# Optimization experiments

Measured on AMD Instinct MI355X. Metric: run time of the kernel, lower is better.

Reference implementation:

```python
import jax, jax.numpy as jnp
import numpy as np

N = 10000
NEG_SLOPE = 0.2

def _glorot(key, shape):
    fan = shape[0] + shape[-1]
    return jax.random.normal(key, shape, dtype=jnp.float32) * jnp.sqrt(2.0 / fan)

def gat_conv(x, src, dst, W, a_src, a_dst, b, heads, ch, concat, n):
    # PyG GATConv: linear (no bias), per-head attention logits, softmax over
    # incoming edges of each target node, weighted scatter-sum, final bias.
    h = (x @ W).reshape(n, heads, ch)                     # [N,H,C]
    al_s = jnp.einsum('nhc,hc->nh', h, a_src)             # [N,H]
    al_d = jnp.einsum('nhc,hc->nh', h, a_dst)
    e = jax.nn.leaky_relu(al_s[src] + al_d[dst], NEG_SLOPE)  # [E,H]
    emax = jax.ops.segment_max(e, dst, num_segments=n)    # [N,H]
    emax = jnp.where(jnp.isfinite(emax), emax, 0.0)
    p = jnp.exp(e - emax[dst])
    denom = jax.ops.segment_sum(p, dst, num_segments=n)   # [N,H]
    alpha = p / (denom[dst] + 1e-16)                      # [E,H]
    out = jax.ops.segment_sum(h[src] * alpha[:, :, None], dst, num_segments=n)
    out = out.reshape(n, heads * ch) if concat else out.mean(axis=1)
    return out + b

def _with_self_loops(edge_index, n):
    loop = jnp.arange(n, dtype=edge_index.dtype)
    src = jnp.concatenate([edge_index[0], loop])
    dst = jnp.concatenate([edge_index[1], loop])
    return src, dst

def setup_inputs() -> dict:
    key = jax.random.key(0)
    ks = jax.random.split(key, 20)
    in_dim, out_dim, E = 128, 256, 160000
    x = jax.random.normal(ks[0], (N, in_dim), dtype=jnp.float32)
    edge_index = jax.random.randint(ks[1], (2, E), 0, N, dtype=jnp.int64)
    return {
        'x': x, 'edge_index': edge_index,
        # conv1: GATConv(128, 256, heads=4, concat=True)
        'W1': _glorot(ks[2], (in_dim, 4 * 256)),
        'a1s': _glorot(ks[3], (4, 256)), 'a1d': _glorot(ks[4], (4, 256)),
        'b1': jnp.zeros((1024,), jnp.float32),
        'S1w': _glorot(ks[5], (in_dim, 1024)), 'S1b': jnp.zeros((1024,), jnp.float32),
        # conv2: GATConv(1024, 256, heads=4, concat=True)
        'W2': _glorot(ks[6], (1024, 4 * 256)),
        'a2s': _glorot(ks[7], (4, 256)), 'a2d': _glorot(ks[8], (4, 256)),
        'b2': jnp.zeros((1024,), jnp.float32),
        'S2w': _glorot(ks[9], (1024, 1024)), 'S2b': jnp.zeros((1024,), jnp.float32),
        # conv3: GATConv(1024, 256, heads=6, concat=False)
        'W3': _glorot(ks[10], (1024, 6 * out_dim)),
        'a3s': _glorot(ks[11], (6, out_dim)), 'a3d': _glorot(ks[12], (6, out_dim)),
        'b3': jnp.zeros((out_dim,), jnp.float32),
        'S3w': _glorot(ks[13], (1024, out_dim)), 'S3b': jnp.zeros((out_dim,), jnp.float32),
    }

def reference(x, edge_index, W1, a1s, a1d, b1, S1w, S1b,
              W2, a2s, a2d, b2, S2w, S2b,
              W3, a3s, a3d, b3, S3w, S3b):
    src, dst = _with_self_loops(edge_index, N)
    h = jax.nn.elu(gat_conv(x, src, dst, W1, a1s, a1d, b1, 4, 256, True, N) + x @ S1w + S1b)
    h = jax.nn.elu(gat_conv(h, src, dst, W2, a2s, a2d, b2, 4, 256, True, N) + h @ S2w + S2b)
    out = gat_conv(h, src, dst, W3, a3s, a3d, b3, 6, 256, False, N) + h @ S3w + S3b
    return out
```

## Files before the change

### kernel.cpp

```cpp
#include <hip/hip_runtime.h>
#include <cfloat>
#include <cmath>
#include <cstdint>

#define NN 10000
#define EE 160000
#define ETOT 170000
#define MPAD 10112

typedef _Float16 f16;
typedef __attribute__((ext_vector_type(8))) _Float16 f16x8;
typedef __attribute__((ext_vector_type(4))) float f32x4;

__global__ __launch_bounds__(256) void count_deg_k(const int* __restrict__ ei,
                                                   int* __restrict__ deg) {
    int e = blockIdx.x * 256 + threadIdx.x;
    if (e < ETOT) {
        int dst = (e < EE) ? ei[EE + e] : (e - EE);
        atomicAdd(&deg[dst], 1);
    }
}

__global__ __launch_bounds__(256) void sc1_k(const int* __restrict__ deg,
                                             int* __restrict__ tmp,
                                             int* __restrict__ bsum) {
    __shared__ int s[256];
    int i = blockIdx.x * 256 + threadIdx.x;
    int v = (i < NN) ? deg[i] : 0;
    s[threadIdx.x] = v;
    __syncthreads();
    for (int d = 1; d < 256; d <<= 1) {
        int t = (threadIdx.x >= d) ? s[threadIdx.x - d] : 0;
        __syncthreads();
        s[threadIdx.x] += t;
        __syncthreads();
    }
    if (i < NN) tmp[i] = s[threadIdx.x];
    if (threadIdx.x == 255) bsum[blockIdx.x] = s[255];
}

__global__ __launch_bounds__(64) void sc2_k(const int* __restrict__ bsum,
                                            int* __restrict__ bbase) {
    int lane = threadIdx.x;
    int v = (lane < 40) ? bsum[lane] : 0;
    int incl = v;
    for (int d = 1; d < 64; d <<= 1) {
        int t = __shfl_up(incl, d, 64);
        if (lane >= d) incl += t;
    }
    if (lane < 40) bbase[lane] = incl - v;
}

__global__ __launch_bounds__(256) void sc3_k(const int* __restrict__ deg,
                                             const int* __restrict__ tmp,
                                             const int* __restrict__ bbase,
                                             int* __restrict__ offs,
                                             int* __restrict__ pos) {
    int i = blockIdx.x * 256 + threadIdx.x;
    if (i < NN) {
        int incl = tmp[i] + bbase[blockIdx.x];
        offs[i + 1] = incl;
        pos[i]      = incl - deg[i];
    }
    if (i == 0) offs[0] = 0;
}

__global__ __launch_bounds__(256) void scatter_k(const int* __restrict__ ei,
                                                 int* __restrict__ pos,
                                                 int* __restrict__ esrc) {
    int e = blockIdx.x * 256 + threadIdx.x;
    if (e < ETOT) {
        int dst = (e < EE) ? ei[EE + e] : (e - EE);
        int src = (e < EE) ? ei[e]      : (e - EE);
        int p = atomicAdd(&pos[dst], 1);
        esrc[p] = src;
    }
}

__device__ __forceinline__ int swz(int r, int ko) { return ko ^ ((r >> 1) & 3); }

template <bool DOELU>
__global__ __launch_bounds__(256) void convA_k(const float* __restrict__ A,
                                               f16* __restrict__ hi,
                                               f16* __restrict__ lo,
                                               int M, int K, int kshift) {
    int idx = blockIdx.x * 256 + threadIdx.x;
    int row = idx >> kshift;
    int kc  = idx & ((1 << kshift) - 1);
    float v[8];
    if (row < M) {
        const float* p = A + (size_t)row * K + kc * 8;
        float4 f0 = *(const float4*)p, f1 = *(const float4*)(p + 4);
        v[0]=f0.x; v[1]=f0.y; v[2]=f0.z; v[3]=f0.w;
        v[4]=f1.x; v[5]=f1.y; v[6]=f1.z; v[7]=f1.w;
        if (DOELU) {
#pragma unroll
            for (int i = 0; i < 8; i++) v[i] = (v[i] > 0.f) ? v[i] : expf(v[i]) - 1.f;
        }
    } else {
#pragma unroll
        for (int i = 0; i < 8; i++) v[i] = 0.f;
    }
    int mblk = row >> 7, r = row & 127;
    int kblk = kc >> 2,  ko = kc & 3;
    int KB = K >> 5;
    size_t off = ((size_t)(mblk * KB + kblk)) * 4096 + r * 32 + swz(r, ko) * 8;
    f16x8 h, l;
#pragma unroll
    for (int i = 0; i < 8; i++) {
        f16 hv = (f16)v[i];
        h[i] = hv;
        l[i] = (f16)(v[i] - (float)hv);
    }
    *(f16x8*)(hi + off) = h;
    *(f16x8*)(lo + off) = l;
}

__global__ __launch_bounds__(256) void convB_k(const float* __restrict__ B,
                                               f16* __restrict__ Bdst,
                                               int NcSrc, int colOff, int KB) {
    int n  = blockIdx.x * 256 + threadIdx.x;
    int kc = blockIdx.y;
    const float* p = B + (size_t)(kc * 8) * NcSrc + n;
    int gcol = colOff + n;
    int nblk = gcol >> 7, r = gcol & 127;
    int kblk = kc >> 2,  ko = kc & 3;
    size_t off = ((size_t)(nblk * KB + kblk)) * 4096 + r * 32 + swz(r, ko) * 8;
    f16x8 h;
#pragma unroll
    for (int i = 0; i < 8; i++) h[i] = (f16)p[(size_t)i * NcSrc];
    *(f16x8*)(Bdst + off) = h;
}

__device__ __forceinline__ void gl_lds16(const void* g, void* l) {
    __builtin_amdgcn_global_load_lds(
        (const __attribute__((address_space(1))) uint32_t*)g,
        (__attribute__((address_space(3))) uint32_t*)l, 16, 0, 0);
}

__global__ __launch_bounds__(256) void mm_k(const f16* __restrict__ Ahi,
                                            const f16* __restrict__ Alo,
                                            const f16* __restrict__ Bhi,
                                            float* __restrict__ C2,
                                            f16* __restrict__ C1h,
                                            const float* __restrict__ bias1,
                                            const float* __restrict__ bias2,
                                            const float* __restrict__ a_s,
                                            const float* __restrict__ a_d,
                                            float* __restrict__ als,
                                            float* __restrict__ ald,
                                            int M, int KB, int NB1,
                                            int N1, int N2, int H) {
    __shared__ __align__(16) char lds[24576];
    const int tid = threadIdx.x;

    const int nwg  = gridDim.x * gridDim.y;
    const int orig = blockIdx.y * gridDim.x + blockIdx.x;
    const int q = nwg >> 3, rr = nwg & 7;
    const int xcd = orig & 7, rk = orig >> 3;
    const int lin = (xcd < rr ? xcd * (q + 1) : rr * (q + 1) + (xcd - rr) * q) + rk;
    const int mblk = lin / gridDim.x, nblk = lin % gridDim.x;

    const int lane = tid & 63, w = tid >> 6;
    const int wr = w >> 1, wc = w & 1;
    const int kg = lane >> 4, l15 = lane & 15;

    int offA[4], offB[4];
#pragma unroll
    for (int t = 0; t < 4; t++) {
        int ra = wr * 64 + t * 16 + l15;
        offA[t] = ra * 64 + swz(ra, kg) * 16;
        int rb = wc * 64 + t * 16 + l15;
        offB[t] = 16384 + rb * 64 + swz(rb, kg) * 16;
    }

    const char* gAh = (const char*)Ahi + (size_t)mblk * KB * 8192;
    const char* gAl = (const char*)Alo + (size_t)mblk * KB * 8192;
    const char* gBh = (const char*)Bhi + (size_t)nblk * KB * 8192;

    f32x4 acc[4][4];
#pragma unroll
    for (int i = 0; i < 4; i++)
#pragma unroll
        for (int j = 0; j < 4; j++) acc[i][j] = (f32x4){0.f, 0.f, 0.f, 0.f};

    for (int kb = 0; kb < KB; kb++) {
        const size_t tk = (size_t)kb * 8192;
        const int t16 = tid * 16;
        gl_lds16(gAh + tk + t16,        lds + t16);
        gl_lds16(gAh + tk + 4096 + t16, lds + 4096 + t16);
        gl_lds16(gAl + tk + t16,        lds + 8192 + t16);
        gl_lds16(gAl + tk + 4096 + t16, lds + 12288 + t16);
        gl_lds16(gBh + tk + t16,        lds + 16384 + t16);
        gl_lds16(gBh + tk + 4096 + t16, lds + 20480 + t16);
        __syncthreads();

        f16x8 ah[4], al[4], b[4];
#pragma unroll
        for (int t = 0; t < 4; t++) {
            ah[t] = *(const f16x8*)(lds + offA[t]);
            al[t] = *(const f16x8*)(lds + 8192 + offA[t]);
            b[t]  = *(const f16x8*)(lds + offB[t]);
        }
#pragma unroll
        for (int i = 0; i < 4; i++)
#pragma unroll
            for (int j = 0; j < 4; j++) {
                acc[i][j] = __builtin_amdgcn_mfma_f32_16x16x32_f16(ah[i], b[j], acc[i][j], 0, 0, 0);
                acc[i][j] = __builtin_amdgcn_mfma_f32_16x16x32_f16(al[i], b[j], acc[i][j], 0, 0, 0);
            }
        __syncthreads();
    }

    const int rowBase = mblk * 128 + wr * 64;
    const int colBase = nblk * 128 + wc * 64;
    if (nblk < NB1) {
#pragma unroll
        for (int i = 0; i < 4; i++)
#pragma unroll
            for (int j = 0; j < 4; j++) {
                int col = colBase + j * 16 + l15;
#pragma unroll
                for (int q2 = 0; q2 < 4; q2++) {
                    int row = rowBase + i * 16 + kg * 4 + q2;
                    C1h[(size_t)row * N1 + col] = (f16)acc[i][j][q2];
                }
            }
        const int head = nblk >> 1;
        const int cIn  = (nblk & 1) * 128 + wc * 64;
        float asv[4], adv[4];
#pragma unroll
        for (int j = 0; j < 4; j++) {
            asv[j] = a_s[head * 256 + cIn + j * 16 + l15];
            adv[j] = a_d[head * 256 + cIn + j * 16 + l15];
        }
#pragma unroll
        for (int i = 0; i < 4; i++)
#pragma unroll
            for (int q2 = 0; q2 < 4; q2++) {
                float vs = acc[i][0][q2] * asv[0] + acc[i][1][q2] * asv[1]
                         + acc[i][2][q2] * asv[2] + acc[i][3][q2] * asv[3];
                float vd = acc[i][0][q2] * adv[0] + acc[i][1][q2] * adv[1]
                         + acc[i][2][q2] * adv[2] + acc[i][3][q2] * adv[3];
                vs += __shfl_xor(vs, 1); vs += __shfl_xor(vs, 2);
                vs += __shfl_xor(vs, 4); vs += __shfl_xor(vs, 8);
                vd += __shfl_xor(vd, 1); vd += __shfl_xor(vd, 2);
                vd += __shfl_xor(vd, 4); vd += __shfl_xor(vd, 8);
                if (l15 == 0) {
                    int row = rowBase + i * 16 + kg * 4 + q2;
                    if (row < M) {
                        atomicAdd(&als[row * H + head], vs);
                        atomicAdd(&ald[row * H + head], vd);
                    }
                }
            }
    } else {
        const int cb2 = NB1 * 128;
#pragma unroll
        for (int i = 0; i < 4; i++)
#pragma unroll
            for (int j = 0; j < 4; j++) {
                int c2 = colBase + j * 16 + l15 - cb2;
                float bsum = bias1[c2] + bias2[c2];
#pragma unroll
                for (int q2 = 0; q2 < 4; q2++) {
                    int row = rowBase + i * 16 + kg * 4 + q2;
                    if (row < M) C2[(size_t)row * N2 + c2] = acc[i][j][q2] + bsum;
                }
            }
    }
}

template <int H, bool MEAN>
__global__ __launch_bounds__(256) void smagg_k(const int* __restrict__ offs,
                                               const int* __restrict__ esrc,
                                               const float* __restrict__ als,
                                               const float* __restrict__ ald,
                                               const f16* __restrict__ hfeat16,
                                               float* __restrict__ out) {
    constexpr int NC = H * 256;
    __shared__ float s_l[128 * 9];
    __shared__ float s_p[128 * 9];
    __shared__ int   s_src[128];
    __shared__ float s_m[8], s_s[8], s_scale[8], s_ad[8];

    const int n = blockIdx.x;
    const int tid = threadIdx.x;
    const int base = offs[n], cnt = offs[n + 1] - base;

    if (tid < H) {
        s_m[tid] = -1e30f;
        s_s[tid] = 0.f;
        s_ad[tid] = ald[n * H + tid];
    }
    float acc[H];
#pragma unroll
    for (int h = 0; h < H; h++) acc[h] = 0.f;
    __syncthreads();

    for (int c0 = 0; c0 < cnt; c0 += 128) {
        const int mcnt = min(128, cnt - c0);
        if (tid < mcnt) {
            int src = esrc[base + c0 + tid];
            s_src[tid] = src;
#pragma unroll
            for (int h = 0; h < H; h++) {
                float l = als[src * H + h] + s_ad[h];
                l = (l < 0.f) ? 0.2f * l : l;
                s_l[tid * 9 + h] = l;
            }
        }
        __syncthreads();
        if (tid < H * 32) {
            int h = tid >> 5, l5 = tid & 31;
            float m = -1e30f;
            for (int e = l5; e < mcnt; e += 32) m = fmaxf(m, s_l[e * 9 + h]);
            for (int o = 16; o > 0; o >>= 1) m = fmaxf(m, __shfl_xor(m, o, 32));
            float mNew = fmaxf(s_m[h], m);
            float ssum = 0.f;
            for (int e = l5; e < mcnt; e += 32) ssum += __expf(s_l[e * 9 + h] - mNew);
            for (int o = 16; o > 0; o >>= 1) ssum += __shfl_xor(ssum, o, 32);
            if (l5 == 0) {
                float scale = __expf(s_m[h] - mNew);
                s_scale[h] = scale;
                s_s[h] = s_s[h] * scale + ssum;
                s_m[h] = mNew;
            }
        }
        __syncthreads();
        if (tid < mcnt) {
#pragma unroll
            for (int h = 0; h < H; h++)
                s_p[tid * 9 + h] = __expf(s_l[tid * 9 + h] - s_m[h]);
        }
#pragma unroll
        for (int h = 0; h < H; h++) acc[h] *= s_scale[h];
        __syncthreads();
        for (int e = 0; e < mcnt; e++) {
            const f16* hp = hfeat16 + (size_t)s_src[e] * NC + tid;
#pragma unroll
            for (int h = 0; h < H; h++)
                acc[h] += s_p[e * 9 + h] * (float)hp[h * 256];
        }
        __syncthreads();
    }

    if (MEAN) {
        float v = 0.f;
#pragma unroll
        for (int h = 0; h < H; h++) v += acc[h] / (s_s[h] + 1e-16f);
        out[(size_t)n * 256 + tid] += v * (1.f / 6.f);
    } else {
#pragma unroll
        for (int h = 0; h < H; h++)
            out[(size_t)n * NC + h * 256 + tid] += acc[h] / (s_s[h] + 1e-16f);
    }
}

extern "C" void kernel_launch(void* const* d_in, const int* in_sizes, int n_in,
                              void* d_out, int out_size, void* d_ws, size_t ws_size,
                              hipStream_t stream) {
    const float* x   = (const float*)d_in[0];
    const int*   ei  = (const int*)d_in[1];
    const float* W1  = (const float*)d_in[2];
    const float* a1s = (const float*)d_in[3];
    const float* a1d = (const float*)d_in[4];
    const float* b1  = (const float*)d_in[5];
    const float* S1w = (const float*)d_in[6];
    const float* S1b = (const float*)d_in[7];
    const float* W2  = (const float*)d_in[8];
    const float* a2s = (const float*)d_in[9];
    const float* a2d = (const float*)d_in[10];
    const float* b2  = (const float*)d_in[11];
    const float* S2w = (const float*)d_in[12];
    const float* S2b = (const float*)d_in[13];
    const float* W3  = (const float*)d_in[14];
    const float* a3s = (const float*)d_in[15];
    const float* a3d = (const float*)d_in[16];
    const float* b3  = (const float*)d_in[17];
    const float* S3w = (const float*)d_in[18];
    const float* S3b = (const float*)d_in[19];
    float* out = (float*)d_out;

    float* ws = (float*)d_ws;
    size_t o = 0;
    float* bufA = ws + o; o += (size_t)NN * 1024;
    float* bufB = ws + o; o += (size_t)NN * 1024;
    float* als  = ws + o; o += (size_t)NN * 6;
    float* ald  = ws + o; o += (size_t)NN * 6;
    f16* hfeat16 = (f16*)(ws + o); o += (size_t)MPAD * 1536 / 2;
    f16* AhiT = (f16*)(ws + o); o += (size_t)MPAD * 1024 / 2;
    f16* AloT = (f16*)(ws + o); o += (size_t)MPAD * 1024 / 2;
    f16* Bt1  = (f16*)(ws + o); o += (size_t)16 * 4  * 4096 / 2;
    f16* Bt2  = (f16*)(ws + o); o += (size_t)16 * 32 * 4096 / 2;
    f16* Bt3  = (f16*)(ws + o); o += (size_t)14 * 32 * 4096 / 2;
    int* deg   = (int*)(ws + o);
    int* tmp   = deg + NN;
    int* bsum  = tmp + NN;
    int* bbase = bsum + 64;
    int* offs  = bbase + 64;
    int* pos   = offs + NN + 1;
    int* esrc  = pos + NN;

    hipMemsetAsync(deg, 0, NN * sizeof(int), stream);
    count_deg_k<<<(ETOT + 255) / 256, 256, 0, stream>>>(ei, deg);
    sc1_k<<<40, 256, 0, stream>>>(deg, tmp, bsum);
    sc2_k<<<1, 64, 0, stream>>>(bsum, bbase);
    sc3_k<<<40, 256, 0, stream>>>(deg, tmp, bbase, offs, pos);
    scatter_k<<<(ETOT + 255) / 256, 256, 0, stream>>>(ei, pos, esrc);

    convB_k<<<dim3(4, 16),  256, 0, stream>>>(W1,  Bt1, 1024, 0,    4);
    convB_k<<<dim3(4, 16),  256, 0, stream>>>(S1w, Bt1, 1024, 1024, 4);
    convB_k<<<dim3(4, 128), 256, 0, stream>>>(W2,  Bt2, 1024, 0,    32);
    convB_k<<<dim3(4, 128), 256, 0, stream>>>(S2w, Bt2, 1024, 1024, 32);
    convB_k<<<dim3(6, 128), 256, 0, stream>>>(W3,  Bt3, 1536, 0,    32);
    convB_k<<<dim3(1, 128), 256, 0, stream>>>(S3w, Bt3, 256,  1536, 32);

    convA_k<false><<<MPAD * 16 / 256, 256, 0, stream>>>(x, AhiT, AloT, NN, 128, 4);
    hipMemsetAsync(als, 0, NN * 12 * sizeof(float), stream);
    mm_k<<<dim3(16, 79), 256, 0, stream>>>(AhiT, AloT, Bt1, bufA, hfeat16, S1b, b1,
                                           a1s, a1d, als, ald,
                                           NN, 4, 8, 1024, 1024, 4);
    smagg_k<4, false><<<NN, 256, 0, stream>>>(offs, esrc, als, ald, hfeat16, bufA);

    convA_k<true><<<MPAD * 128 / 256, 256, 0, stream>>>(bufA, AhiT, AloT, NN, 1024, 7);
    hipMemsetAsync(als, 0, NN * 12 * sizeof(float), stream);
    mm_k<<<dim3(16, 79), 256, 0, stream>>>(AhiT, AloT, Bt2, bufB, hfeat16, S2b, b2,
                                           a2s, a2d, als, ald,
                                           NN, 32, 8, 1024, 1024, 4);
    smagg_k<4, false><<<NN, 256, 0, stream>>>(offs, esrc, als, ald, hfeat16, bufB);

    convA_k<true><<<MPAD * 128 / 256, 256, 0, stream>>>(bufB, AhiT, AloT, NN, 1024, 7);
    hipMemsetAsync(als, 0, NN * 12 * sizeof(float), stream);
    mm_k<<<dim3(14, 79), 256, 0, stream>>>(AhiT, AloT, Bt3, out, hfeat16, S3b, b3,
                                           a3s, a3d, als, ald,
                                           NN, 32, 12, 1536, 256, 6);
    smagg_k<6, true><<<NN, 256, 0, stream>>>(offs, esrc, als, ald, hfeat16, out);
}
```

Baseline: 646.3 us.

## Double-buffer GEMM LDS tiles and fuse ELU plus fp16 split into aggregation

The GEMM kernel now uses two LDS buffers. The next K-block's global-to-LDS loads are issued before computing on the current block, which removes one barrier per iteration and overlaps load latency with MFMA work. The aggregation kernel for layers 1 and 2 now adds the skip/bias output, applies ELU and writes the hi/lo fp16 swizzled A operand directly. This drops the separate convA passes, which read and rewrote the large activation buffer. The cost is twice the LDS per block, which may lower occupancy, and scattered 2-byte stores from the aggregation kernel.

```diff
diff --git a/kernel.cpp b/kernel.cpp
--- a/kernel.cpp
+++ b/kernel.cpp
@@ -138,6 +138,8 @@
         (__attribute__((address_space(3))) uint32_t*)l, 16, 0, 0);
 }
 
+#define MMBUF 24576
+
 __global__ __launch_bounds__(256) void mm_k(const f16* __restrict__ Ahi,
                                             const f16* __restrict__ Alo,
                                             const f16* __restrict__ Bhi,
@@ -151,7 +153,7 @@
                                             float* __restrict__ ald,
                                             int M, int KB, int NB1,
                                             int N1, int N2, int H) {
-    __shared__ __align__(16) char lds[24576];
+    __shared__ __align__(16) char lds[2 * MMBUF];
     const int tid = threadIdx.x;
 
     const int nwg  = gridDim.x * gridDim.y;
@@ -184,23 +186,32 @@
 #pragma unroll
         for (int j = 0; j < 4; j++) acc[i][j] = (f32x4){0.f, 0.f, 0.f, 0.f};
 
+    const int t16 = tid * 16;
+    auto stage = [&](int kb, int buf) {
+        const size_t tk = (size_t)kb * 8192;
+        char* l = lds + buf * MMBUF;
+        gl_lds16(gAh + tk + t16,        l + t16);
+        gl_lds16(gAh + tk + 4096 + t16, l + 4096 + t16);
+        gl_lds16(gAl + tk + t16,        l + 8192 + t16);
+        gl_lds16(gAl + tk + 4096 + t16, l + 12288 + t16);
+        gl_lds16(gBh + tk + t16,        l + 16384 + t16);
+        gl_lds16(gBh + tk + 4096 + t16, l + 20480 + t16);
+    };
+
+    stage(0, 0);
+    __syncthreads();
+
     for (int kb = 0; kb < KB; kb++) {
-        const size_t tk = (size_t)kb * 8192;
-        const int t16 = tid * 16;
-        gl_lds16(gAh + tk + t16,        lds + t16);
-        gl_lds16(gAh + tk + 4096 + t16, lds + 4096 + t16);
-        gl_lds16(gAl + tk + t16,        lds + 8192 + t16);
-        gl_lds16(gAl + tk + 4096 + t16, lds + 12288 + t16);
-        gl_lds16(gBh + tk + t16,        lds + 16384 + t16);
-        gl_lds16(gBh + tk + 4096 + t16, lds + 20480 + t16);
-        __syncthreads();
-
+        const int cur = kb & 1;
+        if (kb + 1 < KB) stage(kb + 1, cur ^ 1);
+
+        const char* l = lds + cur * MMBUF;
         f16x8 ah[4], al[4], b[4];
 #pragma unroll
         for (int t = 0; t < 4; t++) {
-            ah[t] = *(const f16x8*)(lds + offA[t]);
-            al[t] = *(const f16x8*)(lds + 8192 + offA[t]);
-            b[t]  = *(const f16x8*)(lds + offB[t]);
+            ah[t] = *(const f16x8*)(l + offA[t]);
+            al[t] = *(const f16x8*)(l + 8192 + offA[t]);
+            b[t]  = *(const f16x8*)(l + offB[t]);
         }
 #pragma unroll
         for (int i = 0; i < 4; i++)
@@ -277,7 +288,10 @@
                                                const float* __restrict__ als,
                                                const float* __restrict__ ald,
                                                const f16* __restrict__ hfeat16,
-                                               float* __restrict__ out) {
+                                               const float* __restrict__ skipin,
+                                               float* __restrict__ outf,
+                                               f16* __restrict__ hiT,
+                                               f16* __restrict__ loT) {
     constexpr int NC = H * 256;
     __shared__ float s_l[128 * 9];
     __shared__ float s_p[128 * 9];
@@ -349,11 +363,22 @@
         float v = 0.f;
 #pragma unroll
         for (int h = 0; h < H; h++) v += acc[h] / (s_s[h] + 1e-16f);
-        out[(size_t)n * 256 + tid] += v * (1.f / 6.f);
+        outf[(size_t)n * 256 + tid] += v * (1.f / 6.f);
     } else {
-#pragma unroll
-        for (int h = 0; h < H; h++)
-            out[(size_t)n * NC + h * 256 + tid] += acc[h] / (s_s[h] + 1e-16f);
+        const int mblk = n >> 7, r = n & 127;
+#pragma unroll
+        for (int h = 0; h < H; h++) {
+            int c = h * 256 + tid;
+            float v = skipin[(size_t)n * NC + c] + acc[h] / (s_s[h] + 1e-16f);
+            v = (v > 0.f) ? v : expf(v) - 1.f;
+            f16 hv = (f16)v;
+            f16 lv = (f16)(v - (float)hv);
+            int kblk = c >> 5, ko = (c >> 3) & 3;
+            size_t off = ((size_t)(mblk * 32 + kblk)) * 4096
+                       + r * 32 + swz(r, ko) * 8 + (c & 7);
+            hiT[off] = hv;
+            loT[off] = lv;
+        }
     }
 }
 
@@ -421,19 +446,20 @@
     mm_k<<<dim3(16, 79), 256, 0, stream>>>(AhiT, AloT, Bt1, bufA, hfeat16, S1b, b1,
                                            a1s, a1d, als, ald,
                                            NN, 4, 8, 1024, 1024, 4);
-    smagg_k<4, false><<<NN, 256, 0, stream>>>(offs, esrc, als, ald, hfeat16, bufA);
-
-    convA_k<true><<<MPAD * 128 / 256, 256, 0, stream>>>(bufA, AhiT, AloT, NN, 1024, 7);
+    smagg_k<4, false><<<NN, 256, 0, stream>>>(offs, esrc, als, ald, hfeat16,
+                                              bufA, nullptr, AhiT, AloT);
+
     hipMemsetAsync(als, 0, NN * 12 * sizeof(float), stream);
     mm_k<<<dim3(16, 79), 256, 0, stream>>>(AhiT, AloT, Bt2, bufB, hfeat16, S2b, b2,
                                            a2s, a2d, als, ald,
                                            NN, 32, 8, 1024, 1024, 4);
-    smagg_k<4, false><<<NN, 256, 0, stream>>>(offs, esrc, als, ald, hfeat16, bufB);
-
-    convA_k<true><<<MPAD * 128 / 256, 256, 0, stream>>>(bufB, AhiT, AloT, NN, 1024, 7);
+    smagg_k<4, false><<<NN, 256, 0, stream>>>(offs, esrc, als, ald, hfeat16,
+                                              bufB, nullptr, AhiT, AloT);
+
     hipMemsetAsync(als, 0, NN * 12 * sizeof(float), stream);
     mm_k<<<dim3(14, 79), 256, 0, stream>>>(AhiT, AloT, Bt3, out, hfeat16, S3b, b3,
                                            a3s, a3d, als, ald,
                                            NN, 32, 12, 1536, 256, 6);
-    smagg_k<6, true><<<NN, 256, 0, stream>>>(offs, esrc, als, ald, hfeat16, out);
-}
+    smagg_k<6, true><<<NN, 256, 0, stream>>>(offs, esrc, als, ald, hfeat16,
+                                             nullptr, out, nullptr, nullptr);
+}
```

After: 553.6 us. 14.3% less time.
